# Performance work log

Measured on AMD Instinct MI355X. Metric: run time of the kernel, lower is better.

Reference implementation:

```python
import jax, jax.numpy as jnp
import numpy as np

LATENT, INPUT, CLUSTER, N_UNITS = 1024, 512, 256, 100
N_TRAJ, N_TP = 512, 64
# minimum_step = interval/(3*N_TP); uniform spacing dt=1 => n_intermediate_tp = max(2, int(3*N_TP/(N_TP-1))) = 3
N_INTER = 3


def setup_inputs() -> dict:
    key = jax.random.key(0)
    ks = jax.random.split(key, 10)
    d = LATENT + INPUT
    w = lambda k, shp: jax.random.normal(k, shp, jnp.float32) * (shp[0] ** -0.5)
    return {
        "data": jax.random.normal(ks[0], (N_TRAJ, N_TP, INPUT), jnp.float32),
        "time_steps": jnp.arange(N_TP, dtype=jnp.float32),
        "W_u": w(ks[1], (d, LATENT)), "b_u": jnp.zeros((LATENT,), jnp.float32),
        "W_r": w(ks[2], (d, LATENT)), "b_r": jnp.zeros((LATENT,), jnp.float32),
        "W_n": w(ks[3], (d, LATENT)), "b_n": jnp.zeros((LATENT,), jnp.float32),
        "W1": w(ks[4], (LATENT, N_UNITS)), "b1": jnp.zeros((N_UNITS,), jnp.float32),
        "W2": w(ks[5], (N_UNITS, LATENT)), "b2": jnp.zeros((LATENT,), jnp.float32),
        "We": w(ks[6], (LATENT, CLUSTER)), "be": jnp.zeros((CLUSTER,), jnp.float32),
    }


def reference(data, time_steps, W_u, b_u, W_r, b_r, W_n, b_n, W1, b1, W2, b2, We, be):
    # data: [n_traj, n_tp, input]; time_steps: [n_tp]
    def gru_update(y, x):
        yc = jnp.concatenate([y, x], -1)                      # [1, n_traj, latent+input]
        u = jax.nn.sigmoid(yc @ W_u + b_u)                    # update gate
        r = jax.nn.sigmoid(yc @ W_r + b_r)                    # reset gate
        n = jnp.concatenate([y * r, x], -1) @ W_n + b_n       # new state (no nonlinearity in source)
        return (1.0 - u) * n + u * y

    def ode_f(h):
        return jnp.tanh(h @ W1 + b1) @ W2 + b2

    def step(h, inp):
        xi, dt = inp                                          # xi: [1, n_traj, input], dt scalar
        yi_ode = gru_update(h, xi)
        sub = dt / (N_INTER - 1)                              # Euler over linspace(prev_t, t_i, N_INTER)
        def euler(y, _):
            return y + ode_f(y) * sub, None
        y_end, _ = jax.lax.scan(euler, yi_ode, None, length=N_INTER - 1)
        prob = jax.nn.softmax(y_end @ We + be, -1)            # emit_probs
        return y_end, (prob, y_end)

    xs = (jnp.swapaxes(data, 0, 1)[:-1][:, None],             # [n_tp-1, 1, n_traj, input]
          time_steps[1:] - time_steps[:-1])                   # [n_tp-1]
    h0 = jnp.zeros((1, data.shape[0], LATENT), data.dtype)
    _, (probs, states) = jax.lax.scan(step, h0, xs)
    latent_ys = jnp.swapaxes(probs, 0, 1)                     # [1, n_tp-1, n_traj, cluster]
    latent_y_states = jnp.swapaxes(states, 0, 1)              # [1, n_tp-1, n_traj, latent]
    return (latent_ys, latent_y_states)
```

## Files before the change

### kernel.cpp

```cpp
#include <hip/hip_runtime.h>


typedef __bf16 bf16_t;
typedef __bf16 bf16x8 __attribute__((ext_vector_type(8)));
typedef float  f32x4  __attribute__((ext_vector_type(4)));

#define BM 64
#define BN 64
#define BK 64
#define LDT 72

__device__ __forceinline__ float sigmoidf_(float x) { return 1.f / (1.f + expf(-x)); }

__device__ __forceinline__ void split3(float v, bf16_t& h, bf16_t& m, bf16_t& l) {
  h = (bf16_t)v; float r1 = v - (float)h;
  m = (bf16_t)r1; float r2 = r1 - (float)m;
  l = (bf16_t)r2;
}

__device__ __forceinline__ void loadf8(const void* p, size_t idx, int isf32, float out[8]) {
  if (isf32) {
    const float* q = (const float*)p + idx;
    f32x4 a = *(const f32x4*)q;
    f32x4 b = *(const f32x4*)(q + 4);
    out[0]=a[0]; out[1]=a[1]; out[2]=a[2]; out[3]=a[3];
    out[4]=b[0]; out[5]=b[1]; out[6]=b[2]; out[7]=b[3];
  } else {
    bf16x8 v = *(const bf16x8*)((const bf16_t*)p + idx);
#pragma unroll
    for (int i = 0; i < 8; i++) out[i] = (float)v[i];
  }
}
__device__ __forceinline__ float loadf(const void* p, int idx, int isf32) {
  return isf32 ? ((const float*)p)[idx] : (float)((const bf16_t*)p)[idx];
}

__global__ void k_probe(const unsigned int* ts_raw, int* flag) {
  *flag = (ts_raw[0] == 0u) ? 1 : 0;
}

template<bool CATX>
__device__ __forceinline__ void gemm6(
    const bf16_t* __restrict__ Ah, const bf16_t* __restrict__ Am, const bf16_t* __restrict__ Al,
    int lda,
    const void* __restrict__ X, int isf32, int t,
    const bf16_t* __restrict__ Bh, const bf16_t* __restrict__ Bm, const bf16_t* __restrict__ Bl,
    int K,
    f32x4 acc[2][2])
{
  __shared__ __align__(16) bf16_t As[3][BM * LDT];
  __shared__ __align__(16) bf16_t Bs[3][BN * LDT];

  const int tid  = threadIdx.x;
  const int srow = tid >> 2;
  const int sc   = (tid & 3) << 4;
  const int mBase = blockIdx.y * BM;
  const int nBase = blockIdx.x * BN;
  const int arow = mBase + srow;
  const int brow = nBase + srow;

  const int lane = tid & 63;
  const int wid  = tid >> 6;
  const int wm   = (wid & 1) * 32;
  const int wn   = (wid >> 1) * 32;
  const int q8   = (lane >> 4) << 3;
  const int l16  = lane & 15;

  f32x4 z = {0.f, 0.f, 0.f, 0.f};
#pragma unroll
  for (int i = 0; i < 2; i++)
#pragma unroll
    for (int j = 0; j < 2; j++) acc[i][j] = z;

  bf16x8 pA[3][2], pB[3][2];

  auto loadA = [&](int k0) {
    int gk = k0 + sc;
    if (CATX && gk >= 1024) {
      size_t off = (size_t)arow * 32768 + (size_t)t * 512 + (size_t)(gk - 1024);
      float v[16];
      loadf8(X, off,     isf32, v);
      loadf8(X, off + 8, isf32, v + 8);
#pragma unroll
      for (int u8 = 0; u8 < 2; u8++)
#pragma unroll
        for (int j = 0; j < 8; j++) {
          bf16_t h, m, l; split3(v[u8 * 8 + j], h, m, l);
          pA[0][u8][j] = h; pA[1][u8][j] = m; pA[2][u8][j] = l;
        }
    } else {
      size_t off = (size_t)arow * lda + gk;
      pA[0][0] = *(const bf16x8*)(Ah + off); pA[0][1] = *(const bf16x8*)(Ah + off + 8);
      pA[1][0] = *(const bf16x8*)(Am + off); pA[1][1] = *(const bf16x8*)(Am + off + 8);
      pA[2][0] = *(const bf16x8*)(Al + off); pA[2][1] = *(const bf16x8*)(Al + off + 8);
    }
  };
  auto loadB = [&](int k0) {
    size_t off = (size_t)brow * K + k0 + sc;
    pB[0][0] = *(const bf16x8*)(Bh + off); pB[0][1] = *(const bf16x8*)(Bh + off + 8);
    pB[1][0] = *(const bf16x8*)(Bm + off); pB[1][1] = *(const bf16x8*)(Bm + off + 8);
    pB[2][0] = *(const bf16x8*)(Bl + off); pB[2][1] = *(const bf16x8*)(Bl + off + 8);
  };

  loadA(0); loadB(0);

  for (int k0 = 0; k0 < K; k0 += BK) {
    const int wrow = srow * LDT + sc;
#pragma unroll
    for (int p = 0; p < 3; p++) {
      *(bf16x8*)&As[p][wrow]     = pA[p][0];
      *(bf16x8*)&As[p][wrow + 8] = pA[p][1];
      *(bf16x8*)&Bs[p][wrow]     = pB[p][0];
      *(bf16x8*)&Bs[p][wrow + 8] = pB[p][1];
    }
    __syncthreads();

    if (k0 + BK < K) { loadA(k0 + BK); loadB(k0 + BK); }

#pragma unroll
    for (int kk = 0; kk < BK; kk += 32) {
      bf16x8 a[2][3], b[2][3];
#pragma unroll
      for (int p = 0; p < 3; p++) {
        a[0][p] = *(const bf16x8*)&As[p][(wm +      l16) * LDT + kk + q8];
        a[1][p] = *(const bf16x8*)&As[p][(wm + 16 + l16) * LDT + kk + q8];
        b[0][p] = *(const bf16x8*)&Bs[p][(wn +      l16) * LDT + kk + q8];
        b[1][p] = *(const bf16x8*)&Bs[p][(wn + 16 + l16) * LDT + kk + q8];
      }
#pragma unroll
      for (int mi = 0; mi < 2; mi++)
#pragma unroll
        for (int ni = 0; ni < 2; ni++) {
          f32x4 c = acc[mi][ni];
          c = __builtin_amdgcn_mfma_f32_16x16x32_bf16(a[mi][0], b[ni][0], c, 0, 0, 0);
          c = __builtin_amdgcn_mfma_f32_16x16x32_bf16(a[mi][0], b[ni][1], c, 0, 0, 0);
          c = __builtin_amdgcn_mfma_f32_16x16x32_bf16(a[mi][1], b[ni][0], c, 0, 0, 0);
          c = __builtin_amdgcn_mfma_f32_16x16x32_bf16(a[mi][1], b[ni][1], c, 0, 0, 0);
          c = __builtin_amdgcn_mfma_f32_16x16x32_bf16(a[mi][0], b[ni][2], c, 0, 0, 0);
          c = __builtin_amdgcn_mfma_f32_16x16x32_bf16(a[mi][2], b[ni][0], c, 0, 0, 0);
          acc[mi][ni] = c;
        }
    }
    __syncthreads();
  }
}

#define EPI_COORDS \
  const int lane = threadIdx.x & 63; \
  const int wid  = threadIdx.x >> 6; \
  const int row0 = blockIdx.y * BM + (wid & 1) * 32 + ((lane >> 4) << 2); \
  const int col0 = blockIdx.x * BN + (wid >> 1) * 32 + (lane & 15);

__global__ __launch_bounds__(256, 1) void k_gates(
    const bf16_t* __restrict__ hAh, const bf16_t* __restrict__ hAm, const bf16_t* __restrict__ hAl,
    const float* __restrict__ hAf,
    const void* __restrict__ data, int t,
    const bf16_t* __restrict__ Wh, const bf16_t* __restrict__ Wm, const bf16_t* __restrict__ Wl,
    const void* __restrict__ bu, const void* __restrict__ br,
    float* __restrict__ u_f32,
    bf16_t* __restrict__ hrh, bf16_t* __restrict__ hrm, bf16_t* __restrict__ hrl,
    const int* __restrict__ flg)
{
  const int isf32 = *flg;
  f32x4 acc[2][2];
  gemm6<true>(hAh, hAm, hAl, 1024, data, isf32, t, Wh, Wm, Wl, 1536, acc);
  EPI_COORDS
#pragma unroll
  for (int mi = 0; mi < 2; mi++)
#pragma unroll
    for (int ni = 0; ni < 2; ni++)
#pragma unroll
      for (int r = 0; r < 4; r++) {
        int m = row0 + mi * 16 + r;
        int n = col0 + ni * 16;
        float v = acc[mi][ni][r];
        if (n < 1024) {
          u_f32[m * 1024 + n] = sigmoidf_(v + loadf(bu, n, isf32));
        } else {
          int nn = n - 1024;
          float rr = sigmoidf_(v + loadf(br, nn, isf32));
          float hv = hAf[m * 1024 + nn] * rr;
          bf16_t h, mm_, l; split3(hv, h, mm_, l);
          int idx = m * 1024 + nn;
          hrh[idx] = h; hrm[idx] = mm_; hrl[idx] = l;
        }
      }
}

__global__ __launch_bounds__(256, 1) void k_cand(
    const bf16_t* __restrict__ hrh, const bf16_t* __restrict__ hrm, const bf16_t* __restrict__ hrl,
    const void* __restrict__ data, int t,
    const bf16_t* __restrict__ Wh, const bf16_t* __restrict__ Wm, const bf16_t* __restrict__ Wl,
    const void* __restrict__ bn,
    const float* __restrict__ u_f32, const float* __restrict__ h_f32,
    float* __restrict__ h1f,
    bf16_t* __restrict__ h1h, bf16_t* __restrict__ h1m, bf16_t* __restrict__ h1l,
    const int* __restrict__ flg)
{
  const int isf32 = *flg;
  f32x4 acc[2][2];
  gemm6<true>(hrh, hrm, hrl, 1024, data, isf32, t, Wh, Wm, Wl, 1536, acc);
  EPI_COORDS
#pragma unroll
  for (int mi = 0; mi < 2; mi++)
#pragma unroll
    for (int ni = 0; ni < 2; ni++)
#pragma unroll
      for (int r = 0; r < 4; r++) {
        int m = row0 + mi * 16 + r;
        int n = col0 + ni * 16;
        int idx = m * 1024 + n;
        float nv = acc[mi][ni][r] + loadf(bn, n, isf32);
        float u = u_f32[idx];
        float h1 = (1.f - u) * nv + u * h_f32[idx];
        h1 = fminf(fmaxf(h1, -1e6f), 1e6f);
        h1f[idx] = h1;
        bf16_t h, mm_, l; split3(h1, h, mm_, l);
        h1h[idx] = h; h1m[idx] = mm_; h1l[idx] = l;
      }
}

__global__ __launch_bounds__(256, 1) void k_tanh(
    const bf16_t* __restrict__ hh, const bf16_t* __restrict__ hm, const bf16_t* __restrict__ hl,
    const bf16_t* __restrict__ Wh, const bf16_t* __restrict__ Wm, const bf16_t* __restrict__ Wl,
    const void* __restrict__ b1,
    bf16_t* __restrict__ th, bf16_t* __restrict__ tm, bf16_t* __restrict__ tl,
    const int* __restrict__ flg)
{
  const int isf32 = *flg;
  f32x4 acc[2][2];
  gemm6<false>(hh, hm, hl, 1024, nullptr, 0, 0, Wh, Wm, Wl, 1024, acc);
  EPI_COORDS
#pragma unroll
  for (int mi = 0; mi < 2; mi++)
#pragma unroll
    for (int ni = 0; ni < 2; ni++)
#pragma unroll
      for (int r = 0; r < 4; r++) {
        int m = row0 + mi * 16 + r;
        int n = col0 + ni * 16;
        float b = (n < 100) ? loadf(b1, n, isf32) : 0.f;
        float tv = tanhf(acc[mi][ni][r] + b);
        bf16_t h, mm_, l; split3(tv, h, mm_, l);
        int idx = m * 128 + n;
        th[idx] = h; tm[idx] = mm_; tl[idx] = l;
      }
}

template<bool WRITE_STATES>
__global__ __launch_bounds__(256, 1) void k_euler(
    const bf16_t* __restrict__ th, const bf16_t* __restrict__ tm, const bf16_t* __restrict__ tl,
    const bf16_t* __restrict__ Wh, const bf16_t* __restrict__ Wm, const bf16_t* __restrict__ Wl,
    const void* __restrict__ b2, const void* __restrict__ ts, int t,
    const float* __restrict__ hprev_f32,
    float* __restrict__ houtf,
    bf16_t* __restrict__ houth, bf16_t* __restrict__ houtm, bf16_t* __restrict__ houtl,
    float* __restrict__ states, const int* __restrict__ flg)
{
  const int isf32 = *flg;
  f32x4 acc[2][2];
  gemm6<false>(th, tm, tl, 128, nullptr, 0, 0, Wh, Wm, Wl, 128, acc);
  float dt = loadf(ts, t + 1, isf32) - loadf(ts, t, isf32);
  float s = 0.5f * dt;
  EPI_COORDS
#pragma unroll
  for (int mi = 0; mi < 2; mi++)
#pragma unroll
    for (int ni = 0; ni < 2; ni++)
#pragma unroll
      for (int r = 0; r < 4; r++) {
        int m = row0 + mi * 16 + r;
        int n = col0 + ni * 16;
        int idx = m * 1024 + n;
        float hv = hprev_f32[idx] + s * (acc[mi][ni][r] + loadf(b2, n, isf32));
        hv = fminf(fmaxf(hv, -1e6f), 1e6f);
        houtf[idx] = hv;
        bf16_t h, mm_, l; split3(hv, h, mm_, l);
        houth[idx] = h; houtm[idx] = mm_; houtl[idx] = l;
        if (WRITE_STATES)
          states[((size_t)t * 512 + m) * 1024 + n] = hv;
      }
}

__global__ __launch_bounds__(256, 1) void k_emit(
    const bf16_t* __restrict__ hh, const bf16_t* __restrict__ hm, const bf16_t* __restrict__ hl,
    const bf16_t* __restrict__ Wh, const bf16_t* __restrict__ Wm, const bf16_t* __restrict__ Wl,
    const void* __restrict__ be, float* __restrict__ logits, const int* __restrict__ flg)
{
  const int isf32 = *flg;
  f32x4 acc[2][2];
  gemm6<false>(hh, hm, hl, 1024, nullptr, 0, 0, Wh, Wm, Wl, 1024, acc);
  EPI_COORDS
#pragma unroll
  for (int mi = 0; mi < 2; mi++)
#pragma unroll
    for (int ni = 0; ni < 2; ni++)
#pragma unroll
      for (int r = 0; r < 4; r++) {
        int m = row0 + mi * 16 + r;
        int n = col0 + ni * 16;
        logits[m * 256 + n] = acc[mi][ni][r] + loadf(be, n, isf32);
      }
}

__global__ __launch_bounds__(256) void k_softmax(
    const float* __restrict__ logits, float* __restrict__ probs, int t)
{
  int m = blockIdx.x;
  int j = threadIdx.x;
  float v = logits[m * 256 + j];
  __shared__ float red[256];
  red[j] = v;
  __syncthreads();
  for (int s = 128; s > 0; s >>= 1) {
    if (j < s) red[j] = fmaxf(red[j], red[j + s]);
    __syncthreads();
  }
  float mx = red[0];
  __syncthreads();
  float e = expf(v - mx);
  red[j] = e;
  __syncthreads();
  for (int s = 128; s > 0; s >>= 1) {
    if (j < s) red[j] += red[j + s];
    __syncthreads();
  }
  probs[((size_t)t * 512 + m) * 256 + j] = e / red[0];
}

__global__ void k_transpose_split(const void* __restrict__ src,
                                  bf16_t* __restrict__ dh, bf16_t* __restrict__ dm,
                                  bf16_t* __restrict__ dl,
                                  int K, int N, int Kpad, const int* __restrict__ flg)
{
  const int isf32 = *flg;
  int k = blockIdx.x * 256 + threadIdx.x;
  if (k >= Kpad) return;
  int n = blockIdx.y;
  float v = 0.f;
  if (k < K && n < N) v = loadf(src, k * N + n, isf32);
  bf16_t h, m, l; split3(v, h, m, l);
  size_t idx = (size_t)n * Kpad + k;
  dh[idx] = h; dm[idx] = m; dl[idx] = l;
}

extern "C" void kernel_launch(void* const* d_in, const int* in_sizes, int n_in,
                              void* d_out, int out_size, void* d_ws, size_t ws_size,
                              hipStream_t stream) {
  const void* data = d_in[0];
  const void* ts   = d_in[1];
  const void* Wu   = d_in[2];
  const void* bu   = d_in[3];
  const void* Wr   = d_in[4];
  const void* br   = d_in[5];
  const void* Wn   = d_in[6];
  const void* bn   = d_in[7];
  const void* W1   = d_in[8];
  const void* b1   = d_in[9];
  const void* W2   = d_in[10];
  const void* b2   = d_in[11];
  const void* We   = d_in[12];
  const void* be   = d_in[13];

  float* out_probs  = (float*)d_out;
  float* out_states = (float*)d_out + (size_t)63 * 512 * 256;

  char* p = (char*)d_ws;
  auto carve = [&](size_t bytes) { char* r = p; p += (bytes + 255) & ~255ull; return (void*)r; };
  int*    flg   = (int*)carve(256);
  bf16_t* WurTh = (bf16_t*)carve((size_t)2048 * 1536 * 2);
  bf16_t* WurTm = (bf16_t*)carve((size_t)2048 * 1536 * 2);
  bf16_t* WurTl = (bf16_t*)carve((size_t)2048 * 1536 * 2);
  bf16_t* WnTh  = (bf16_t*)carve((size_t)1024 * 1536 * 2);
  bf16_t* WnTm  = (bf16_t*)carve((size_t)1024 * 1536 * 2);
  bf16_t* WnTl  = (bf16_t*)carve((size_t)1024 * 1536 * 2);
  bf16_t* W1Th  = (bf16_t*)carve((size_t)128 * 1024 * 2);
  bf16_t* W1Tm  = (bf16_t*)carve((size_t)128 * 1024 * 2);
  bf16_t* W1Tl  = (bf16_t*)carve((size_t)128 * 1024 * 2);
  bf16_t* W2Th  = (bf16_t*)carve((size_t)1024 * 128 * 2);
  bf16_t* W2Tm  = (bf16_t*)carve((size_t)1024 * 128 * 2);
  bf16_t* W2Tl  = (bf16_t*)carve((size_t)1024 * 128 * 2);
  bf16_t* WeTh  = (bf16_t*)carve((size_t)256 * 1024 * 2);
  bf16_t* WeTm  = (bf16_t*)carve((size_t)256 * 1024 * 2);
  bf16_t* WeTl  = (bf16_t*)carve((size_t)256 * 1024 * 2);
  float*  P0f = (float*)carve((size_t)512 * 1024 * 4);
  float*  P1f = (float*)carve((size_t)512 * 1024 * 4);
  float*  P2f = (float*)carve((size_t)512 * 1024 * 4);
  bf16_t* P0h = (bf16_t*)carve((size_t)512 * 1024 * 2);
  bf16_t* P0m = (bf16_t*)carve((size_t)512 * 1024 * 2);
  bf16_t* P0l = (bf16_t*)carve((size_t)512 * 1024 * 2);
  bf16_t* P1h = (bf16_t*)carve((size_t)512 * 1024 * 2);
  bf16_t* P1m = (bf16_t*)carve((size_t)512 * 1024 * 2);
  bf16_t* P1l = (bf16_t*)carve((size_t)512 * 1024 * 2);
  bf16_t* P2h = (bf16_t*)carve((size_t)512 * 1024 * 2);
  bf16_t* P2m = (bf16_t*)carve((size_t)512 * 1024 * 2);
  bf16_t* P2l = (bf16_t*)carve((size_t)512 * 1024 * 2);
  bf16_t* HRh = (bf16_t*)carve((size_t)512 * 1024 * 2);
  bf16_t* HRm = (bf16_t*)carve((size_t)512 * 1024 * 2);
  bf16_t* HRl = (bf16_t*)carve((size_t)512 * 1024 * 2);
  float*  uf  = (float*)carve((size_t)512 * 1024 * 4);
  bf16_t* Th  = (bf16_t*)carve((size_t)512 * 128 * 2);
  bf16_t* Tm  = (bf16_t*)carve((size_t)512 * 128 * 2);
  bf16_t* Tl  = (bf16_t*)carve((size_t)512 * 128 * 2);
  float*  lg  = (float*)carve((size_t)512 * 256 * 4);

  (void)hipMemsetAsync(P0f, 0, (size_t)512 * 1024 * 4, stream);
  (void)hipMemsetAsync(P0h, 0, (size_t)512 * 1024 * 2, stream);
  (void)hipMemsetAsync(P0m, 0, (size_t)512 * 1024 * 2, stream);
  (void)hipMemsetAsync(P0l, 0, (size_t)512 * 1024 * 2, stream);

  dim3 b256(256);
  k_probe<<<1, 1, 0, stream>>>((const unsigned int*)ts, flg);

  k_transpose_split<<<dim3(6, 1024), b256, 0, stream>>>(Wu, WurTh, WurTm, WurTl, 1536, 1024, 1536, flg);
  k_transpose_split<<<dim3(6, 1024), b256, 0, stream>>>(Wr, WurTh + (size_t)1024 * 1536,
                                                        WurTm + (size_t)1024 * 1536,
                                                        WurTl + (size_t)1024 * 1536, 1536, 1024, 1536, flg);
  k_transpose_split<<<dim3(6, 1024), b256, 0, stream>>>(Wn, WnTh, WnTm, WnTl, 1536, 1024, 1536, flg);
  k_transpose_split<<<dim3(4, 128),  b256, 0, stream>>>(W1, W1Th, W1Tm, W1Tl, 1024, 100, 1024, flg);
  k_transpose_split<<<dim3(1, 1024), b256, 0, stream>>>(W2, W2Th, W2Tm, W2Tl, 100, 1024, 128, flg);
  k_transpose_split<<<dim3(4, 256),  b256, 0, stream>>>(We, WeTh, WeTm, WeTl, 1024, 256, 1024, flg);

  for (int t = 0; t < 63; t++) {
    k_gates<<<dim3(32, 8), b256, 0, stream>>>(P0h, P0m, P0l, P0f, data, t,
                                              WurTh, WurTm, WurTl, bu, br,
                                              uf, HRh, HRm, HRl, flg);
    k_cand <<<dim3(16, 8), b256, 0, stream>>>(HRh, HRm, HRl, data, t,
                                              WnTh, WnTm, WnTl, bn, uf, P0f,
                                              P1f, P1h, P1m, P1l, flg);
    k_tanh <<<dim3(2, 8),  b256, 0, stream>>>(P1h, P1m, P1l, W1Th, W1Tm, W1Tl, b1,
                                              Th, Tm, Tl, flg);
    k_euler<false><<<dim3(16, 8), b256, 0, stream>>>(Th, Tm, Tl, W2Th, W2Tm, W2Tl, b2, ts, t,
                                                     P1f, P2f, P2h, P2m, P2l, nullptr, flg);
    k_tanh <<<dim3(2, 8),  b256, 0, stream>>>(P2h, P2m, P2l, W1Th, W1Tm, W1Tl, b1,
                                              Th, Tm, Tl, flg);
    k_euler<true> <<<dim3(16, 8), b256, 0, stream>>>(Th, Tm, Tl, W2Th, W2Tm, W2Tl, b2, ts, t,
                                                     P2f, P0f, P0h, P0m, P0l, out_states, flg);
    k_emit <<<dim3(4, 8),  b256, 0, stream>>>(P0h, P0m, P0l, WeTh, WeTm, WeTl, be, lg, flg);
    k_softmax<<<512, b256, 0, stream>>>(lg, out_probs, t);
  }
}
```

Before: 11.01 ms.

## Fuse per-timestep kernel chain into one persistent kernel with grid barriers

Replaces the 8 kernel launches per timestep (504 total) with a single persistent kernel of 256 blocks. Stages are separated by a software grid barrier built on atomics. The emit GEMM for step t-1 is overlapped with the gates stage of step t, and the softmax for t-1 is overlapped with the candidate stage. This is meant to remove launch overhead and idle tails between the small GEMMs. The cost is spin-wait barriers, idle blocks in the narrow stages, and reliance on all 256 blocks being co-resident; if they are not, the barrier can deadlock.

```diff
diff --git a/kernel.cpp b/kernel.cpp
--- a/kernel.cpp
+++ b/kernel.cpp
@@ -9,6 +9,7 @@
 #define BN 64
 #define BK 64
 #define LDT 72
+#define NBLK 256
 
 __device__ __forceinline__ float sigmoidf_(float x) { return 1.f / (1.f + expf(-x)); }
 
@@ -17,6 +18,14 @@
   m = (bf16_t)r1; float r2 = r1 - (float)m;
   l = (bf16_t)r2;
 }
+
+#define CHAIN6(c, ah, am, al, bh, bm, bl) \
+  c = __builtin_amdgcn_mfma_f32_16x16x32_bf16(ah, bh, c, 0, 0, 0); \
+  c = __builtin_amdgcn_mfma_f32_16x16x32_bf16(ah, bm, c, 0, 0, 0); \
+  c = __builtin_amdgcn_mfma_f32_16x16x32_bf16(am, bh, c, 0, 0, 0); \
+  c = __builtin_amdgcn_mfma_f32_16x16x32_bf16(am, bm, c, 0, 0, 0); \
+  c = __builtin_amdgcn_mfma_f32_16x16x32_bf16(ah, bl, c, 0, 0, 0); \
+  c = __builtin_amdgcn_mfma_f32_16x16x32_bf16(al, bh, c, 0, 0, 0);
 
 __device__ __forceinline__ void loadf8(const void* p, size_t idx, int isf32, float out[8]) {
   if (isf32) {
@@ -39,23 +48,36 @@
   *flag = (ts_raw[0] == 0u) ? 1 : 0;
 }
 
+__device__ __forceinline__ void gbar(int* bar) {
+  __syncthreads();
+  if (threadIdx.x == 0) {
+    int g = __hip_atomic_load(bar + 16, __ATOMIC_RELAXED, __HIP_MEMORY_SCOPE_AGENT);
+    int old = __hip_atomic_fetch_add(bar, 1, __ATOMIC_ACQ_REL, __HIP_MEMORY_SCOPE_AGENT);
+    if (old == NBLK - 1) {
+      __hip_atomic_store(bar, 0, __ATOMIC_RELAXED, __HIP_MEMORY_SCOPE_AGENT);
+      __hip_atomic_fetch_add(bar + 16, 1, __ATOMIC_RELEASE, __HIP_MEMORY_SCOPE_AGENT);
+    } else {
+      while (__hip_atomic_load(bar + 16, __ATOMIC_ACQUIRE, __HIP_MEMORY_SCOPE_AGENT) == g) {
+        __builtin_amdgcn_s_sleep(8);
+      }
+    }
+  }
+  __syncthreads();
+}
+
 template<bool CATX>
-__device__ __forceinline__ void gemm6(
+__device__ __forceinline__ void gemm6_dev(
+    bf16_t* __restrict__ AsB, bf16_t* __restrict__ BsB,
     const bf16_t* __restrict__ Ah, const bf16_t* __restrict__ Am, const bf16_t* __restrict__ Al,
     int lda,
     const void* __restrict__ X, int isf32, int t,
     const bf16_t* __restrict__ Bh, const bf16_t* __restrict__ Bm, const bf16_t* __restrict__ Bl,
-    int K,
+    int K, int mBase, int nBase,
     f32x4 acc[2][2])
 {
-  __shared__ __align__(16) bf16_t As[3][BM * LDT];
-  __shared__ __align__(16) bf16_t Bs[3][BN * LDT];
-
   const int tid  = threadIdx.x;
   const int srow = tid >> 2;
   const int sc   = (tid & 3) << 4;
-  const int mBase = blockIdx.y * BM;
-  const int nBase = blockIdx.x * BN;
   const int arow = mBase + srow;
   const int brow = nBase + srow;
 
@@ -108,10 +130,10 @@
     const int wrow = srow * LDT + sc;
 #pragma unroll
     for (int p = 0; p < 3; p++) {
-      *(bf16x8*)&As[p][wrow]     = pA[p][0];
-      *(bf16x8*)&As[p][wrow + 8] = pA[p][1];
-      *(bf16x8*)&Bs[p][wrow]     = pB[p][0];
-      *(bf16x8*)&Bs[p][wrow + 8] = pB[p][1];
+      *(bf16x8*)&AsB[p * (BM * LDT) + wrow]     = pA[p][0];
+      *(bf16x8*)&AsB[p * (BM * LDT) + wrow + 8] = pA[p][1];
+      *(bf16x8*)&BsB[p * (BN * LDT) + wrow]     = pB[p][0];
+      *(bf16x8*)&BsB[p * (BN * LDT) + wrow + 8] = pB[p][1];
     }
     __syncthreads();
 
@@ -122,22 +144,17 @@
       bf16x8 a[2][3], b[2][3];
 #pragma unroll
       for (int p = 0; p < 3; p++) {
-        a[0][p] = *(const bf16x8*)&As[p][(wm +      l16) * LDT + kk + q8];
-        a[1][p] = *(const bf16x8*)&As[p][(wm + 16 + l16) * LDT + kk + q8];
-        b[0][p] = *(const bf16x8*)&Bs[p][(wn +      l16) * LDT + kk + q8];
-        b[1][p] = *(const bf16x8*)&Bs[p][(wn + 16 + l16) * LDT + kk + q8];
+        a[0][p] = *(const bf16x8*)&AsB[p * (BM * LDT) + (wm +      l16) * LDT + kk + q8];
+        a[1][p] = *(const bf16x8*)&AsB[p * (BM * LDT) + (wm + 16 + l16) * LDT + kk + q8];
+        b[0][p] = *(const bf16x8*)&BsB[p * (BN * LDT) + (wn +      l16) * LDT + kk + q8];
+        b[1][p] = *(const bf16x8*)&BsB[p * (BN * LDT) + (wn + 16 + l16) * LDT + kk + q8];
       }
 #pragma unroll
       for (int mi = 0; mi < 2; mi++)
 #pragma unroll
         for (int ni = 0; ni < 2; ni++) {
           f32x4 c = acc[mi][ni];
-          c = __builtin_amdgcn_mfma_f32_16x16x32_bf16(a[mi][0], b[ni][0], c, 0, 0, 0);
-          c = __builtin_amdgcn_mfma_f32_16x16x32_bf16(a[mi][0], b[ni][1], c, 0, 0, 0);
-          c = __builtin_amdgcn_mfma_f32_16x16x32_bf16(a[mi][1], b[ni][0], c, 0, 0, 0);
-          c = __builtin_amdgcn_mfma_f32_16x16x32_bf16(a[mi][1], b[ni][1], c, 0, 0, 0);
-          c = __builtin_amdgcn_mfma_f32_16x16x32_bf16(a[mi][0], b[ni][2], c, 0, 0, 0);
-          c = __builtin_amdgcn_mfma_f32_16x16x32_bf16(a[mi][2], b[ni][0], c, 0, 0, 0);
+          CHAIN6(c, a[mi][0], a[mi][1], a[mi][2], b[ni][0], b[ni][1], b[ni][2]);
           acc[mi][ni] = c;
         }
     }
@@ -145,187 +162,211 @@
   }
 }
 
-#define EPI_COORDS \
-  const int lane = threadIdx.x & 63; \
-  const int wid  = threadIdx.x >> 6; \
-  const int row0 = blockIdx.y * BM + (wid & 1) * 32 + ((lane >> 4) << 2); \
-  const int col0 = blockIdx.x * BN + (wid >> 1) * 32 + (lane & 15);
-
-__global__ __launch_bounds__(256, 1) void k_gates(
-    const bf16_t* __restrict__ hAh, const bf16_t* __restrict__ hAm, const bf16_t* __restrict__ hAl,
-    const float* __restrict__ hAf,
-    const void* __restrict__ data, int t,
-    const bf16_t* __restrict__ Wh, const bf16_t* __restrict__ Wm, const bf16_t* __restrict__ Wl,
-    const void* __restrict__ bu, const void* __restrict__ br,
-    float* __restrict__ u_f32,
-    bf16_t* __restrict__ hrh, bf16_t* __restrict__ hrm, bf16_t* __restrict__ hrl,
-    const int* __restrict__ flg)
+struct KArgs {
+  const void* data; const void* ts;
+  const void* bu; const void* br; const void* bn;
+  const void* b1; const void* b2; const void* be;
+  const bf16_t *WurTh, *WurTm, *WurTl;
+  const bf16_t *WnTh,  *WnTm,  *WnTl;
+  const bf16_t *W1Th,  *W1Tm,  *W1Tl;
+  const bf16_t *W2Th,  *W2Tm,  *W2Tl;
+  const bf16_t *WeTh,  *WeTm,  *WeTl;
+  float *P0f, *P1f, *P2f, *uf, *lg;
+  bf16_t *P0h, *P0m, *P0l;
+  bf16_t *P1h, *P1m, *P1l;
+  bf16_t *P2h, *P2m, *P2l;
+  bf16_t *HRh, *HRm, *HRl;
+  bf16_t *Th,  *Tm,  *Tl;
+  float *states, *probs;
+  const int* flg;
+  int* bar;
+};
+
+__global__ __launch_bounds__(256, 1) void k_mega(KArgs a)
 {
-  const int isf32 = *flg;
-  f32x4 acc[2][2];
-  gemm6<true>(hAh, hAm, hAl, 1024, data, isf32, t, Wh, Wm, Wl, 1536, acc);
-  EPI_COORDS
-#pragma unroll
-  for (int mi = 0; mi < 2; mi++)
-#pragma unroll
-    for (int ni = 0; ni < 2; ni++)
-#pragma unroll
-      for (int r = 0; r < 4; r++) {
-        int m = row0 + mi * 16 + r;
-        int n = col0 + ni * 16;
-        float v = acc[mi][ni][r];
-        if (n < 1024) {
-          u_f32[m * 1024 + n] = sigmoidf_(v + loadf(bu, n, isf32));
-        } else {
-          int nn = n - 1024;
-          float rr = sigmoidf_(v + loadf(br, nn, isf32));
-          float hv = hAf[m * 1024 + nn] * rr;
-          bf16_t h, mm_, l; split3(hv, h, mm_, l);
-          int idx = m * 1024 + nn;
-          hrh[idx] = h; hrm[idx] = mm_; hrl[idx] = l;
+  __shared__ __align__(16) bf16_t AsB[3 * BM * LDT];
+  __shared__ __align__(16) bf16_t BsB[3 * BN * LDT];
+
+  const int bid  = blockIdx.x;
+  const int tid  = threadIdx.x;
+  const int lane = tid & 63;
+  const int wid  = tid >> 6;
+  const int isf32 = *a.flg;
+
+  auto emit_tile = [&]() {
+    const int mt = bid >> 2, nt = bid & 3;
+    f32x4 acc[2][2];
+    gemm6_dev<false>(AsB, BsB, a.P0h, a.P0m, a.P0l, 1024, nullptr, 0, 0,
+                     a.WeTh, a.WeTm, a.WeTl, 1024, mt * BM, nt * BN, acc);
+    const int row0 = mt * BM + (wid & 1) * 32 + ((lane >> 4) << 2);
+    const int col0 = nt * BN + (wid >> 1) * 32 + (lane & 15);
+#pragma unroll
+    for (int mi = 0; mi < 2; mi++)
+#pragma unroll
+      for (int ni = 0; ni < 2; ni++)
+#pragma unroll
+        for (int r = 0; r < 4; r++) {
+          int m = row0 + mi * 16 + r;
+          int n = col0 + ni * 16;
+          a.lg[m * 256 + n] = acc[mi][ni][r] + loadf(a.be, n, isf32);
         }
+  };
+
+  auto softmax_rows = [&](int sb, int t) {
+    float* red = (float*)AsB;
+#pragma unroll
+    for (int rr = 0; rr < 4; ++rr) {
+      int m = sb * 4 + rr;
+      float v = a.lg[m * 256 + tid];
+      red[tid] = v;
+      __syncthreads();
+      for (int s = 128; s > 0; s >>= 1) {
+        if (tid < s) red[tid] = fmaxf(red[tid], red[tid + s]);
+        __syncthreads();
       }
-}
-
-__global__ __launch_bounds__(256, 1) void k_cand(
-    const bf16_t* __restrict__ hrh, const bf16_t* __restrict__ hrm, const bf16_t* __restrict__ hrl,
-    const void* __restrict__ data, int t,
-    const bf16_t* __restrict__ Wh, const bf16_t* __restrict__ Wm, const bf16_t* __restrict__ Wl,
-    const void* __restrict__ bn,
-    const float* __restrict__ u_f32, const float* __restrict__ h_f32,
-    float* __restrict__ h1f,
-    bf16_t* __restrict__ h1h, bf16_t* __restrict__ h1m, bf16_t* __restrict__ h1l,
-    const int* __restrict__ flg)
-{
-  const int isf32 = *flg;
-  f32x4 acc[2][2];
-  gemm6<true>(hrh, hrm, hrl, 1024, data, isf32, t, Wh, Wm, Wl, 1536, acc);
-  EPI_COORDS
-#pragma unroll
-  for (int mi = 0; mi < 2; mi++)
-#pragma unroll
-    for (int ni = 0; ni < 2; ni++)
-#pragma unroll
-      for (int r = 0; r < 4; r++) {
-        int m = row0 + mi * 16 + r;
-        int n = col0 + ni * 16;
-        int idx = m * 1024 + n;
-        float nv = acc[mi][ni][r] + loadf(bn, n, isf32);
-        float u = u_f32[idx];
-        float h1 = (1.f - u) * nv + u * h_f32[idx];
-        h1 = fminf(fmaxf(h1, -1e6f), 1e6f);
-        h1f[idx] = h1;
-        bf16_t h, mm_, l; split3(h1, h, mm_, l);
-        h1h[idx] = h; h1m[idx] = mm_; h1l[idx] = l;
+      float mx = red[0];
+      __syncthreads();
+      float e = expf(v - mx);
+      red[tid] = e;
+      __syncthreads();
+      for (int s = 128; s > 0; s >>= 1) {
+        if (tid < s) red[tid] += red[tid + s];
+        __syncthreads();
       }
-}
-
-__global__ __launch_bounds__(256, 1) void k_tanh(
-    const bf16_t* __restrict__ hh, const bf16_t* __restrict__ hm, const bf16_t* __restrict__ hl,
-    const bf16_t* __restrict__ Wh, const bf16_t* __restrict__ Wm, const bf16_t* __restrict__ Wl,
-    const void* __restrict__ b1,
-    bf16_t* __restrict__ th, bf16_t* __restrict__ tm, bf16_t* __restrict__ tl,
-    const int* __restrict__ flg)
-{
-  const int isf32 = *flg;
-  f32x4 acc[2][2];
-  gemm6<false>(hh, hm, hl, 1024, nullptr, 0, 0, Wh, Wm, Wl, 1024, acc);
-  EPI_COORDS
-#pragma unroll
-  for (int mi = 0; mi < 2; mi++)
-#pragma unroll
-    for (int ni = 0; ni < 2; ni++)
-#pragma unroll
-      for (int r = 0; r < 4; r++) {
-        int m = row0 + mi * 16 + r;
-        int n = col0 + ni * 16;
-        float b = (n < 100) ? loadf(b1, n, isf32) : 0.f;
-        float tv = tanhf(acc[mi][ni][r] + b);
-        bf16_t h, mm_, l; split3(tv, h, mm_, l);
-        int idx = m * 128 + n;
-        th[idx] = h; tm[idx] = mm_; tl[idx] = l;
-      }
-}
-
-template<bool WRITE_STATES>
-__global__ __launch_bounds__(256, 1) void k_euler(
-    const bf16_t* __restrict__ th, const bf16_t* __restrict__ tm, const bf16_t* __restrict__ tl,
-    const bf16_t* __restrict__ Wh, const bf16_t* __restrict__ Wm, const bf16_t* __restrict__ Wl,
-    const void* __restrict__ b2, const void* __restrict__ ts, int t,
-    const float* __restrict__ hprev_f32,
-    float* __restrict__ houtf,
-    bf16_t* __restrict__ houth, bf16_t* __restrict__ houtm, bf16_t* __restrict__ houtl,
-    float* __restrict__ states, const int* __restrict__ flg)
-{
-  const int isf32 = *flg;
-  f32x4 acc[2][2];
-  gemm6<false>(th, tm, tl, 128, nullptr, 0, 0, Wh, Wm, Wl, 128, acc);
-  float dt = loadf(ts, t + 1, isf32) - loadf(ts, t, isf32);
-  float s = 0.5f * dt;
-  EPI_COORDS
-#pragma unroll
-  for (int mi = 0; mi < 2; mi++)
-#pragma unroll
-    for (int ni = 0; ni < 2; ni++)
-#pragma unroll
-      for (int r = 0; r < 4; r++) {
-        int m = row0 + mi * 16 + r;
-        int n = col0 + ni * 16;
-        int idx = m * 1024 + n;
-        float hv = hprev_f32[idx] + s * (acc[mi][ni][r] + loadf(b2, n, isf32));
-        hv = fminf(fmaxf(hv, -1e6f), 1e6f);
-        houtf[idx] = hv;
-        bf16_t h, mm_, l; split3(hv, h, mm_, l);
-        houth[idx] = h; houtm[idx] = mm_; houtl[idx] = l;
-        if (WRITE_STATES)
-          states[((size_t)t * 512 + m) * 1024 + n] = hv;
-      }
-}
-
-__global__ __launch_bounds__(256, 1) void k_emit(
-    const bf16_t* __restrict__ hh, const bf16_t* __restrict__ hm, const bf16_t* __restrict__ hl,
-    const bf16_t* __restrict__ Wh, const bf16_t* __restrict__ Wm, const bf16_t* __restrict__ Wl,
-    const void* __restrict__ be, float* __restrict__ logits, const int* __restrict__ flg)
-{
-  const int isf32 = *flg;
-  f32x4 acc[2][2];
-  gemm6<false>(hh, hm, hl, 1024, nullptr, 0, 0, Wh, Wm, Wl, 1024, acc);
-  EPI_COORDS
-#pragma unroll
-  for (int mi = 0; mi < 2; mi++)
-#pragma unroll
-    for (int ni = 0; ni < 2; ni++)
-#pragma unroll
-      for (int r = 0; r < 4; r++) {
-        int m = row0 + mi * 16 + r;
-        int n = col0 + ni * 16;
-        logits[m * 256 + n] = acc[mi][ni][r] + loadf(be, n, isf32);
-      }
-}
-
-__global__ __launch_bounds__(256) void k_softmax(
-    const float* __restrict__ logits, float* __restrict__ probs, int t)
-{
-  int m = blockIdx.x;
-  int j = threadIdx.x;
-  float v = logits[m * 256 + j];
-  __shared__ float red[256];
-  red[j] = v;
-  __syncthreads();
-  for (int s = 128; s > 0; s >>= 1) {
-    if (j < s) red[j] = fmaxf(red[j], red[j + s]);
-    __syncthreads();
+      a.probs[((size_t)t * 512 + m) * 256 + tid] = e / red[0];
+      __syncthreads();
+    }
+  };
+
+  for (int t = 0; t < 63; ++t) {
+    const float sdt = 0.5f * (loadf(a.ts, t + 1, isf32) - loadf(a.ts, t, isf32));
+
+    {
+      const int mt = bid >> 5, nt = bid & 31;
+      f32x4 acc[2][2];
+      gemm6_dev<true>(AsB, BsB, a.P0h, a.P0m, a.P0l, 1024, a.data, isf32, t,
+                      a.WurTh, a.WurTm, a.WurTl, 1536, mt * BM, nt * BN, acc);
+      const int row0 = mt * BM + (wid & 1) * 32 + ((lane >> 4) << 2);
+      const int col0 = nt * BN + (wid >> 1) * 32 + (lane & 15);
+#pragma unroll
+      for (int mi = 0; mi < 2; mi++)
+#pragma unroll
+        for (int ni = 0; ni < 2; ni++)
+#pragma unroll
+          for (int r = 0; r < 4; r++) {
+            int m = row0 + mi * 16 + r;
+            int n = col0 + ni * 16;
+            float v = acc[mi][ni][r];
+            if (n < 1024) {
+              a.uf[m * 1024 + n] = sigmoidf_(v + loadf(a.bu, n, isf32));
+            } else {
+              int nn = n - 1024;
+              float rr = sigmoidf_(v + loadf(a.br, nn, isf32));
+              float hv = a.P0f[m * 1024 + nn] * rr;
+              bf16_t h, mm_, l; split3(hv, h, mm_, l);
+              int idx = m * 1024 + nn;
+              a.HRh[idx] = h; a.HRm[idx] = mm_; a.HRl[idx] = l;
+            }
+          }
+      if (t > 0 && bid < 32) emit_tile();
+    }
+    gbar(a.bar);
+
+    if (bid < 128) {
+      const int mt = bid >> 4, nt = bid & 15;
+      f32x4 acc[2][2];
+      gemm6_dev<true>(AsB, BsB, a.HRh, a.HRm, a.HRl, 1024, a.data, isf32, t,
+                      a.WnTh, a.WnTm, a.WnTl, 1536, mt * BM, nt * BN, acc);
+      const int row0 = mt * BM + (wid & 1) * 32 + ((lane >> 4) << 2);
+      const int col0 = nt * BN + (wid >> 1) * 32 + (lane & 15);
+#pragma unroll
+      for (int mi = 0; mi < 2; mi++)
+#pragma unroll
+        for (int ni = 0; ni < 2; ni++)
+#pragma unroll
+          for (int r = 0; r < 4; r++) {
+            int m = row0 + mi * 16 + r;
+            int n = col0 + ni * 16;
+            int idx = m * 1024 + n;
+            float nv = acc[mi][ni][r] + loadf(a.bn, n, isf32);
+            float u = a.uf[idx];
+            float h1 = (1.f - u) * nv + u * a.P0f[idx];
+            h1 = fminf(fmaxf(h1, -1e6f), 1e6f);
+            a.P1f[idx] = h1;
+            bf16_t h, mm_, l; split3(h1, h, mm_, l);
+            a.P1h[idx] = h; a.P1m[idx] = mm_; a.P1l[idx] = l;
+          }
+    } else if (t > 0) {
+      softmax_rows(bid - 128, t - 1);
+    }
+    gbar(a.bar);
+
+    auto stage_tanh = [&](const bf16_t* sh, const bf16_t* sm, const bf16_t* sl) {
+      const int mt = bid >> 1, nt = bid & 1;
+      f32x4 acc[2][2];
+      gemm6_dev<false>(AsB, BsB, sh, sm, sl, 1024, nullptr, 0, 0,
+                       a.W1Th, a.W1Tm, a.W1Tl, 1024, mt * BM, nt * BN, acc);
+      const int row0 = mt * BM + (wid & 1) * 32 + ((lane >> 4) << 2);
+      const int col0 = nt * BN + (wid >> 1) * 32 + (lane & 15);
+#pragma unroll
+      for (int mi = 0; mi < 2; mi++)
+#pragma unroll
+        for (int ni = 0; ni < 2; ni++)
+#pragma unroll
+          for (int r = 0; r < 4; r++) {
+            int m = row0 + mi * 16 + r;
+            int n = col0 + ni * 16;
+            float b = (n < 100) ? loadf(a.b1, n, isf32) : 0.f;
+            float tv = tanhf(acc[mi][ni][r] + b);
+            bf16_t h, mm_, l; split3(tv, h, mm_, l);
+            int idx = m * 128 + n;
+            a.Th[idx] = h; a.Tm[idx] = mm_; a.Tl[idx] = l;
+          }
+    };
+
+    auto stage_euler = [&](const float* hprev, float* houtf,
+                           bf16_t* hoh, bf16_t* hom, bf16_t* hol, bool wrS) {
+      const int mt = bid >> 4, nt = bid & 15;
+      f32x4 acc[2][2];
+      gemm6_dev<false>(AsB, BsB, a.Th, a.Tm, a.Tl, 128, nullptr, 0, 0,
+                       a.W2Th, a.W2Tm, a.W2Tl, 128, mt * BM, nt * BN, acc);
+      const int row0 = mt * BM + (wid & 1) * 32 + ((lane >> 4) << 2);
+      const int col0 = nt * BN + (wid >> 1) * 32 + (lane & 15);
+#pragma unroll
+      for (int mi = 0; mi < 2; mi++)
+#pragma unroll
+        for (int ni = 0; ni < 2; ni++)
+#pragma unroll
+          for (int r = 0; r < 4; r++) {
+            int m = row0 + mi * 16 + r;
+            int n = col0 + ni * 16;
+            int idx = m * 1024 + n;
+            float hv = hprev[idx] + sdt * (acc[mi][ni][r] + loadf(a.b2, n, isf32));
+            hv = fminf(fmaxf(hv, -1e6f), 1e6f);
+            houtf[idx] = hv;
+            bf16_t h, mm_, l; split3(hv, h, mm_, l);
+            hoh[idx] = h; hom[idx] = mm_; hol[idx] = l;
+            if (wrS)
+              a.states[((size_t)t * 512 + m) * 1024 + n] = hv;
+          }
+    };
+
+    if (bid < 16) stage_tanh(a.P1h, a.P1m, a.P1l);
+    gbar(a.bar);
+
+    if (bid < 128) stage_euler(a.P1f, a.P2f, a.P2h, a.P2m, a.P2l, false);
+    gbar(a.bar);
+
+    if (bid < 16) stage_tanh(a.P2h, a.P2m, a.P2l);
+    gbar(a.bar);
+
+    if (bid < 128) stage_euler(a.P2f, a.P0f, a.P0h, a.P0m, a.P0l, true);
+    gbar(a.bar);
   }
-  float mx = red[0];
-  __syncthreads();
-  float e = expf(v - mx);
-  red[j] = e;
-  __syncthreads();
-  for (int s = 128; s > 0; s >>= 1) {
-    if (j < s) red[j] += red[j + s];
-    __syncthreads();
-  }
-  probs[((size_t)t * 512 + m) * 256 + j] = e / red[0];
+
+  if (bid < 32) emit_tile();
+  gbar(a.bar);
+  if (bid < 128) softmax_rows(bid, 62);
 }
 
 __global__ void k_transpose_split(const void* __restrict__ src,
@@ -368,6 +409,7 @@
   char* p = (char*)d_ws;
   auto carve = [&](size_t bytes) { char* r = p; p += (bytes + 255) & ~255ull; return (void*)r; };
   int*    flg   = (int*)carve(256);
+  int*    bar   = (int*)carve(256);
   bf16_t* WurTh = (bf16_t*)carve((size_t)2048 * 1536 * 2);
   bf16_t* WurTm = (bf16_t*)carve((size_t)2048 * 1536 * 2);
   bf16_t* WurTl = (bf16_t*)carve((size_t)2048 * 1536 * 2);
@@ -408,6 +450,7 @@
   (void)hipMemsetAsync(P0h, 0, (size_t)512 * 1024 * 2, stream);
   (void)hipMemsetAsync(P0m, 0, (size_t)512 * 1024 * 2, stream);
   (void)hipMemsetAsync(P0l, 0, (size_t)512 * 1024 * 2, stream);
+  (void)hipMemsetAsync(bar, 0, 256, stream);
 
   dim3 b256(256);
   k_probe<<<1, 1, 0, stream>>>((const unsigned int*)ts, flg);
@@ -421,22 +464,23 @@
   k_transpose_split<<<dim3(1, 1024), b256, 0, stream>>>(W2, W2Th, W2Tm, W2Tl, 100, 1024, 128, flg);
   k_transpose_split<<<dim3(4, 256),  b256, 0, stream>>>(We, WeTh, WeTm, WeTl, 1024, 256, 1024, flg);
 
-  for (int t = 0; t < 63; t++) {
-    k_gates<<<dim3(32, 8), b256, 0, stream>>>(P0h, P0m, P0l, P0f, data, t,
-                                              WurTh, WurTm, WurTl, bu, br,
-                                              uf, HRh, HRm, HRl, flg);
-    k_cand <<<dim3(16, 8), b256, 0, stream>>>(HRh, HRm, HRl, data, t,
-                                              WnTh, WnTm, WnTl, bn, uf, P0f,
-                                              P1f, P1h, P1m, P1l, flg);
-    k_tanh <<<dim3(2, 8),  b256, 0, stream>>>(P1h, P1m, P1l, W1Th, W1Tm, W1Tl, b1,
-                                              Th, Tm, Tl, flg);
-    k_euler<false><<<dim3(16, 8), b256, 0, stream>>>(Th, Tm, Tl, W2Th, W2Tm, W2Tl, b2, ts, t,
-                                                     P1f, P2f, P2h, P2m, P2l, nullptr, flg);
-    k_tanh <<<dim3(2, 8),  b256, 0, stream>>>(P2h, P2m, P2l, W1Th, W1Tm, W1Tl, b1,
-                                              Th, Tm, Tl, flg);
-    k_euler<true> <<<dim3(16, 8), b256, 0, stream>>>(Th, Tm, Tl, W2Th, W2Tm, W2Tl, b2, ts, t,
-                                                     P2f, P0f, P0h, P0m, P0l, out_states, flg);
-    k_emit <<<dim3(4, 8),  b256, 0, stream>>>(P0h, P0m, P0l, WeTh, WeTm, WeTl, be, lg, flg);
-    k_softmax<<<512, b256, 0, stream>>>(lg, out_probs, t);
-  }
-}
+  KArgs ha;
+  ha.data = data; ha.ts = ts;
+  ha.bu = bu; ha.br = br; ha.bn = bn; ha.b1 = b1; ha.b2 = b2; ha.be = be;
+  ha.WurTh = WurTh; ha.WurTm = WurTm; ha.WurTl = WurTl;
+  ha.WnTh = WnTh;   ha.WnTm = WnTm;   ha.WnTl = WnTl;
+  ha.W1Th = W1Th;   ha.W1Tm = W1Tm;   ha.W1Tl = W1Tl;
+  ha.W2Th = W2Th;   ha.W2Tm = W2Tm;   ha.W2Tl = W2Tl;
+  ha.WeTh = WeTh;   ha.WeTm = WeTm;   ha.WeTl = WeTl;
+  ha.P0f = P0f; ha.P1f = P1f; ha.P2f = P2f; ha.uf = uf; ha.lg = lg;
+  ha.P0h = P0h; ha.P0m = P0m; ha.P0l = P0l;
+  ha.P1h = P1h; ha.P1m = P1m; ha.P1l = P1l;
+  ha.P2h = P2h; ha.P2m = P2m; ha.P2l = P2l;
+  ha.HRh = HRh; ha.HRm = HRm; ha.HRl = HRl;
+  ha.Th = Th; ha.Tm = Tm; ha.Tl = Tl;
+  ha.states = out_states; ha.probs = out_probs;
+  ha.flg = flg;
+  ha.bar = bar;
+
+  k_mega<<<dim3(NBLK), b256, 0, stream>>>(ha);
+}
```

Result: slower. 38.24 ms (+247.3%).
